# Kernel optimization log

Hardware: AMD Instinct MI355X
Metric: run time of the kernel (lower is better)

Reference implementation:

```python
import jax, jax.numpy as jnp
from jax import lax
import numpy as np

TAU = 10.0      # tauSr == tauRef
THR = 1.0       # theta
WIDTH = 1.0     # tauRho (surrogate width)
SCALE = 1.0     # scaleRho (surrogate scale)
DECAY = float(np.exp(-1.0 / TAU))


@jax.custom_vjp
def _heaviside(v):
    # spike = 1[v >= theta]
    return (v >= THR).astype(v.dtype)

def _heaviside_fwd(v):
    return _heaviside(v), v

def _heaviside_bwd(v, g):
    # SLAYER exponential surrogate pdf: scaleRho/tauRho * exp(-|v-theta|/tauRho)
    return (g * (SCALE / WIDTH) * jnp.exp(-jnp.abs(v - THR) / WIDTH),)

_heaviside.defvjp(_heaviside_fwd, _heaviside_bwd)


def _conv2d(x, w, pad):
    # x: (B, Cin, H, W), w: (Cout, Cin, kh, kw); SLAYER convs have no bias
    return lax.conv_general_dilated(
        x, w, window_strides=(1, 1), padding=[(pad, pad), (pad, pad)],
        dimension_numbers=("NCHW", "OIHW", "NCHW"))


def _sumpool(x, k):
    # SLAYER pool = sum over kxk window (times a learned scalar applied outside)
    B, C, H, W = x.shape
    return x.reshape(B, C, H // k, k, W // k, k).sum(axis=(3, 5))


def _psp(seq):
    # exponential synaptic (PSP) filter along time: s[t] = a*s[t-1] + x[t]
    a = jnp.asarray(DECAY, seq.dtype)
    def step(s, x_t):
        s = a * s + x_t
        return s, s
    _, out = lax.scan(step, jnp.zeros_like(seq[0]), seq)
    return out  # (T, ...)


def _spikes(u):
    # thresholded spiking with decaying refractory feedback (scaleRef=1):
    # v[t] = u[t] - r[t]; s[t] = 1[v >= theta]; r[t+1] = b*(r[t] + theta*s[t])
    b = jnp.asarray(DECAY, u.dtype)
    def step(r, u_t):
        s = _heaviside(u_t - r)
        r_next = b * (r + THR * s)
        return r_next, s
    _, out = lax.scan(step, jnp.zeros_like(u[0]), u)
    return out  # (T, ...)


def _forward(x, conv1_w, conv2_w, lin_w, w_pool1, w_pool2):
    N, T, C, H, W = x.shape  # (64, 100, 2, 32, 32)
    h = _conv2d(x.reshape(N * T, C, H, W), conv1_w, 2)        # (NT, 4, 32, 32)
    h = _sumpool(h, 4) * w_pool1                               # (NT, 4, 8, 8)
    h = h.reshape(N, T, 4, 8, 8).swapaxes(0, 1)                # (T, N, 4, 8, 8)
    s1 = _spikes(_psp(h))                                      # (T, N, 4, 8, 8)
    h2 = _conv2d(s1.reshape(T * N, 4, 8, 8), conv2_w, 1)       # (TN, 8, 8, 8)
    h2 = (_sumpool(h2, 2) * w_pool2).reshape(T, N, 8, 4, 4)    # (T, N, 8, 4, 4)
    s2 = _spikes(_psp(h2))                                     # (T, N, 8, 4, 4)
    # dense = full-spatial conv (2, 8, 4, 4) -> (N, T, 2)
    return jnp.einsum("tnchw,ochw->nto", s2, lin_w)


def setup_inputs() -> dict:
    key = jax.random.key(0)
    ks = jax.random.split(key, 4)
    x = (jax.random.uniform(ks[0], (64, 100, 2, 32, 32)) < 0.1).astype(jnp.float32)
    conv1_w = jax.random.normal(ks[1], (4, 2, 5, 5), jnp.float32) * 0.3
    conv2_w = jax.random.normal(ks[2], (8, 4, 3, 3), jnp.float32) * 0.3
    lin_w = jax.random.normal(ks[3], (2, 8, 4, 4), jnp.float32) * 0.3
    w_pool1 = jnp.float32(1.0 / 16.0)  # 1.1*theta / (16 * 1.1)
    w_pool2 = jnp.float32(1.0 / 4.0)   # 1.1*theta / (4 * 1.1)
    return {"x": x, "conv1_w": conv1_w, "conv2_w": conv2_w, "lin_w": lin_w,
            "w_pool1": w_pool1, "w_pool2": w_pool2}


def reference(x, conv1_w, conv2_w, lin_w, w_pool1, w_pool2):
    return _forward(x, conv1_w, conv2_w, lin_w, w_pool1, w_pool2)
```

## Files before the change

kernel.cpp:

```cpp
#include <hip/hip_runtime.h>


#define DECAY 0.9048374180359595f

__global__ __launch_bounds__(128) void k0_fold(const float* __restrict__ w1,
        const float* __restrict__ w2, const float* __restrict__ wp1,
        const float* __restrict__ wp2, float* __restrict__ wl1,
        float* __restrict__ wl2) {
    const int tid = threadIdx.x;
    const float p1 = wp1[0], p2 = wp2[0];
    for (int idx = tid; idx < 512; idx += 128) {
        const int f = idx & 7, c = (idx >> 3) & 3, e = (idx >> 5) & 7, cin = idx >> 8;
        const int cc = c * 2 + cin;
        int alo = e - 3; if (alo < 0) alo = 0;
        int ahi = e;     if (ahi > 4) ahi = 4;
        int blo = f - 3; if (blo < 0) blo = 0;
        int bhi = f;     if (bhi > 4) bhi = 4;
        float s = 0.f;
        for (int a = alo; a <= ahi; ++a)
            for (int b = blo; b <= bhi; ++b)
                s += w1[cc * 25 + a * 5 + b];
        wl1[(cin * 8 + e) * 32 + c * 8 + f] = s * p1;
    }
    for (int idx = tid; idx < 512; idx += 128) {
        const int c2 = idx & 7, f = (idx >> 3) & 3, e = (idx >> 5) & 3, cin = idx >> 7;
        int alo = e - 1; if (alo < 0) alo = 0;
        int ahi = e;     if (ahi > 2) ahi = 2;
        int blo = f - 1; if (blo < 0) blo = 0;
        int bhi = f;     if (bhi > 2) bhi = 2;
        float s = 0.f;
        for (int aa = alo; aa <= ahi; ++aa)
            for (int bb = blo; bb <= bhi; ++bb)
                s += w2[((c2 * 4 + cin) * 3 + aa) * 3 + bb];
        wl2[c2 * 68 + cin * 16 + e * 4 + f] = s * p2;
    }
}

__global__ __launch_bounds__(64) void k1(const float* __restrict__ x,
        const float* __restrict__ wg, float* __restrict__ u1) {
    __shared__ __align__(16) float xs[2 * 1296];
    __shared__ __align__(16) float wl[512];
    const int lane = threadIdx.x;
    const int frame = blockIdx.x;
    const int n = frame / 100, t = frame % 100;

    *(float4*)(wl + 4 * lane)       = *(const float4*)(wg + 4 * lane);
    *(float4*)(wl + 256 + 4 * lane) = *(const float4*)(wg + 256 + 4 * lane);

    #pragma unroll
    for (int m0 = 0; m0 < 128; m0 += 64) {
        const int m = m0 + lane;
        if (m < 72) {
            const int cin = m / 36, rem = m % 36;
            const int rr = rem / 9, q4 = rem % 9;
            const int pr = (rr == 0) ? 0 : (rr == 1) ? 9 : (rr == 2) ? 26 : 35;
            *(float4*)(xs + cin * 1296 + pr * 36 + q4 * 4) = make_float4(0.f, 0.f, 0.f, 0.f);
        }
    }
    #pragma unroll
    for (int m0 = 0; m0 < 192; m0 += 64) {
        const int m = m0 + lane;
        if (m < 144) {
            const int cin = m / 72, rem = m % 72;
            const int side = rem & 1, pr = rem >> 1;
            *(float2*)(xs + cin * 1296 + pr * 36 + side * 34) = make_float2(0.f, 0.f);
        }
    }
    const float4* xg = (const float4*)(x + (size_t)frame * 2048);
    #pragma unroll
    for (int q = 0; q < 8; ++q) {
        const int m = q * 64 + lane;
        const float4 v = xg[m];
        const int li = 4 * m;
        const int cin = li >> 10, row = (li >> 5) & 31, col = li & 31;
        const int r = row + 2;
        const int pr = (r & 3) * 9 + (r >> 2);
        float* d = xs + cin * 1296 + pr * 36 + col + 2;
        *(float2*)(d)     = make_float2(v.x, v.y);
        *(float2*)(d + 2) = make_float2(v.z, v.w);
    }
    __syncthreads();

    const int cp = lane >> 5;
    const int i  = (lane >> 2) & 7;
    const int jh = (lane >> 1) & 1;
    const int eh = lane & 1;

    float acc[2][4] = {{0.f, 0.f, 0.f, 0.f}, {0.f, 0.f, 0.f, 0.f}};
    const float* tb = xs + (i + eh) * 36 + jh * 16;
    #pragma unroll
    for (int cin = 0; cin < 2; ++cin) {
        #pragma unroll
        for (int et = 0; et < 4; ++et) {
            const int ro = cin * 1296 + et * 9 * 36;
            float xr[20];
            #pragma unroll
            for (int b = 0; b < 5; ++b)
                *(float4*)(xr + 4 * b) = *(const float4*)(tb + ro + 4 * b);
            float wv[16];
            const float* wp = wl + (cin * 8 + eh * 4 + et) * 32 + cp * 16;
            #pragma unroll
            for (int q = 0; q < 4; ++q)
                *(float4*)(wv + 4 * q) = *(const float4*)(wp + 4 * q);
            #pragma unroll
            for (int cl = 0; cl < 2; ++cl) {
                #pragma unroll
                for (int jj = 0; jj < 4; ++jj) {
                    const int o = 4 * jj;
                    acc[cl][jj] += xr[o]*wv[cl*8]     + xr[o+1]*wv[cl*8+1]
                                 + xr[o+2]*wv[cl*8+2] + xr[o+3]*wv[cl*8+3]
                                 + xr[o+4]*wv[cl*8+4] + xr[o+5]*wv[cl*8+5]
                                 + xr[o+6]*wv[cl*8+6] + xr[o+7]*wv[cl*8+7];
                }
            }
        }
    }
    #pragma unroll
    for (int cl = 0; cl < 2; ++cl)
        #pragma unroll
        for (int jj = 0; jj < 4; ++jj)
            acc[cl][jj] += __shfl_xor(acc[cl][jj], 1);

    const float o0 = eh ? acc[1][0] : acc[0][0];
    const float o1 = eh ? acc[1][1] : acc[0][1];
    const float o2 = eh ? acc[1][2] : acc[0][2];
    const float o3 = eh ? acc[1][3] : acc[0][3];
    *(float4*)(u1 + (size_t)t * 16384 + n * 256 + (2 * cp + eh) * 64 + i * 8 + jh * 4) =
        make_float4(o0, o1, o2, o3);
}

__global__ __launch_bounds__(64) void k2_scan(float* __restrict__ u) {
    const int id = blockIdx.x * 64 + threadIdx.x;
    const float a = DECAY;
    float* p = u + id;
    float v[100];
    #pragma unroll
    for (int k = 0; k < 100; ++k) v[k] = p[(size_t)k * 16384];
    float psp = 0.f, r = 0.f;
    #pragma unroll
    for (int k = 0; k < 100; ++k) {
        psp = a * psp + v[k];
        const float vv = psp - r;
        const float s = (vv >= 1.f) ? 1.f : 0.f;
        r = a * (r + s);
        p[(size_t)k * 16384] = s;
    }
}

__global__ __launch_bounds__(256) void k3(const float* __restrict__ s1,
        const float* __restrict__ wl2g, float* __restrict__ u2) {
    __shared__ __align__(16) float xs[8 * 660];
    __shared__ __align__(16) float wl[544];
    const int tid = threadIdx.x, sub = tid >> 5, l = tid & 31;

    for (int m = tid; m < 136; m += 256)
        *(float4*)(wl + 4 * m) = *(const float4*)(wl2g + 4 * m);

    float* xt = xs + sub * 660;
    float4* fz = (float4*)xt;
    for (int m = l; m < 160; m += 32) fz[m] = make_float4(0.f, 0.f, 0.f, 0.f);

    const int frame = blockIdx.x * 8 + sub;
    const int t = frame >> 6, n = frame & 63;
    const float* fr = s1 + (size_t)t * 16384 + n * 256;
    {
        const int cin = l >> 3, row = l & 7;
        const int r = row + 1;
        const int pr = (r & 1) * 5 + (r >> 1);
        const float4 v0 = *(const float4*)(fr + cin * 64 + row * 8);
        const float4 v1 = *(const float4*)(fr + cin * 64 + row * 8 + 4);
        *(float4*)(xt + cin * 160 + pr * 16 + 4) = v0;
        *(float4*)(xt + cin * 160 + pr * 16 + 8) = v1;
    }
    __syncthreads();

    const int c2 = l >> 2, i = l & 3;
    float acc[4] = {0.f, 0.f, 0.f, 0.f};
    const float* wb = wl + c2 * 68;
    const float* tb = xt + i * 16;
    #pragma unroll
    for (int cin = 0; cin < 4; ++cin) {
        #pragma unroll
        for (int e = 0; e < 4; ++e) {
            const int C = cin * 160 + ((e & 1) * 5 + (e >> 1)) * 16;
            float xr[16];
            #pragma unroll
            for (int b = 0; b < 4; ++b)
                *(float4*)(xr + 4 * b) = *(const float4*)(tb + C + 4 * b);
            float wv[4];
            *(float4*)(wv) = *(const float4*)(wb + cin * 16 + e * 4);
            #pragma unroll
            for (int j = 0; j < 4; ++j) {
                #pragma unroll
                for (int f = 0; f < 4; ++f)
                    acc[j] += xr[2 * j + f + 3] * wv[f];
            }
        }
    }
    *(float4*)(u2 + (size_t)t * 8192 + n * 128 + c2 * 16 + i * 4) =
        make_float4(acc[0], acc[1], acc[2], acc[3]);
}

__global__ __launch_bounds__(128, 2) void k45(const float* __restrict__ u2,
        const float* __restrict__ lw, float* __restrict__ out) {
    __shared__ float ls[25 * 128];
    const int f = threadIdx.x, n = blockIdx.x;
    const int wave = f >> 6, l = f & 63;
    const float a = DECAY;
    const float w0 = lw[l], w1v = lw[64 + l], w2v = lw[128 + l], w3v = lw[192 + l];
    float psp = 0.f, r = 0.f;
    const float* p = u2 + n * 128 + f;
    #pragma unroll 1
    for (int t0 = 0; t0 < 100; t0 += 25) {
        float v[25];
        #pragma unroll
        for (int k = 0; k < 25; ++k) v[k] = p[(size_t)(t0 + k) * 8192];
        #pragma unroll
        for (int k = 0; k < 25; ++k) {
            psp = a * psp + v[k];
            const float vv = psp - r;
            const float s = (vv >= 1.f) ? 1.f : 0.f;
            r = a * (r + s);
            ls[k * 128 + f] = s;
        }
        __syncthreads();
        const int base = wave ? 13 : 0, cnt = wave ? 12 : 13;
        for (int q = 0; q < cnt; ++q) {
            const int k = base + q;
            const float sa = ls[k * 128 + l], sb = ls[k * 128 + 64 + l];
            float a0 = sa * w0 + sb * w1v;
            float a1 = sa * w2v + sb * w3v;
            #pragma unroll
            for (int off = 32; off > 0; off >>= 1) {
                a0 += __shfl_down(a0, off);
                a1 += __shfl_down(a1, off);
            }
            if (l == 0) {
                const int tt = t0 + k;
                out[n * 200 + tt * 2]     = a0;
                out[n * 200 + tt * 2 + 1] = a1;
            }
        }
        __syncthreads();
    }
}

extern "C" void kernel_launch(void* const* d_in, const int* in_sizes, int n_in,
                              void* d_out, int out_size, void* d_ws, size_t ws_size,
                              hipStream_t stream) {
    const float* x   = (const float*)d_in[0];
    const float* w1  = (const float*)d_in[1];
    const float* w2  = (const float*)d_in[2];
    const float* lw  = (const float*)d_in[3];
    const float* wp1 = (const float*)d_in[4];
    const float* wp2 = (const float*)d_in[5];

    float* u1  = (float*)d_ws;
    float* u2  = u1 + 1638400;
    float* wl1 = u2 + 819200;
    float* wl2 = wl1 + 512;
    float* out = (float*)d_out;

    k0_fold<<<1, 128, 0, stream>>>(w1, w2, wp1, wp2, wl1, wl2);
    k1<<<6400, 64, 0, stream>>>(x, wl1, u1);
    k2_scan<<<256, 64, 0, stream>>>(u1);
    k3<<<800, 256, 0, stream>>>(u1, wl2, u2);
    k45<<<64, 128, 0, stream>>>(u2, lw, out);
}
```

Before: 140.6 us.

## Fuse first scan, second conv, second scan and dense layer into one kernel

Replaces k2_scan, k3 and k45 with a single kernel kf that runs one block per batch sample and walks time in chunks of 8 steps. In each chunk it computes the first PSP and spike scan, runs the 3x3 conv on spikes held in shared memory, then the second scan and the dense reduction. This removes the s1 write-back, the u2 round trip through global memory and two launches, and it prefetches the next chunk of u1 into registers. The cost is that the whole tail now runs on only 64 blocks with several barriers per chunk, so parallelism and latency hiding are much lower than in the 800-block conv kernel.

```diff
diff --git a/kernel.cpp b/kernel.cpp
--- a/kernel.cpp
+++ b/kernel.cpp
@@ -129,116 +129,126 @@
         make_float4(o0, o1, o2, o3);
 }
 
-__global__ __launch_bounds__(64) void k2_scan(float* __restrict__ u) {
-    const int id = blockIdx.x * 64 + threadIdx.x;
+__global__ __launch_bounds__(256) void kf(const float* __restrict__ u1,
+        const float* __restrict__ wl2g, const float* __restrict__ lw,
+        float* __restrict__ out) {
+    __shared__ __align__(16) float ls1[8 * 660];
+    __shared__ __align__(16) float ls2[8 * 132];
+    __shared__ __align__(16) float wl[544];
+    const int tid = threadIdx.x, n = blockIdx.x;
+    const int wave = tid >> 6, l64 = tid & 63;
+    const int sub = tid >> 5, l = tid & 31;
     const float a = DECAY;
-    float* p = u + id;
-    float v[100];
-    #pragma unroll
-    for (int k = 0; k < 100; ++k) v[k] = p[(size_t)k * 16384];
-    float psp = 0.f, r = 0.f;
-    #pragma unroll
-    for (int k = 0; k < 100; ++k) {
-        psp = a * psp + v[k];
-        const float vv = psp - r;
-        const float s = (vv >= 1.f) ? 1.f : 0.f;
-        r = a * (r + s);
-        p[(size_t)k * 16384] = s;
-    }
-}
-
-__global__ __launch_bounds__(256) void k3(const float* __restrict__ s1,
-        const float* __restrict__ wl2g, float* __restrict__ u2) {
-    __shared__ __align__(16) float xs[8 * 660];
-    __shared__ __align__(16) float wl[544];
-    const int tid = threadIdx.x, sub = tid >> 5, l = tid & 31;
-
-    for (int m = tid; m < 136; m += 256)
-        *(float4*)(wl + 4 * m) = *(const float4*)(wl2g + 4 * m);
-
-    float* xt = xs + sub * 660;
-    float4* fz = (float4*)xt;
-    for (int m = l; m < 160; m += 32) fz[m] = make_float4(0.f, 0.f, 0.f, 0.f);
-
-    const int frame = blockIdx.x * 8 + sub;
-    const int t = frame >> 6, n = frame & 63;
-    const float* fr = s1 + (size_t)t * 16384 + n * 256;
-    {
-        const int cin = l >> 3, row = l & 7;
-        const int r = row + 1;
-        const int pr = (r & 1) * 5 + (r >> 1);
-        const float4 v0 = *(const float4*)(fr + cin * 64 + row * 8);
-        const float4 v1 = *(const float4*)(fr + cin * 64 + row * 8 + 4);
-        *(float4*)(xt + cin * 160 + pr * 16 + 4) = v0;
-        *(float4*)(xt + cin * 160 + pr * 16 + 8) = v1;
-    }
+
+    if (tid < 136) *(float4*)(wl + 4 * tid) = *(const float4*)(wl2g + 4 * tid);
+    for (int m = tid; m < 1320; m += 256)
+        *(float4*)(ls1 + 4 * m) = make_float4(0.f, 0.f, 0.f, 0.f);
+
+    const int cs = tid >> 6, rowi = (tid >> 3) & 7, col = tid & 7;
+    const int pr1 = (((rowi + 1) & 1) * 5) + ((rowi + 1) >> 1);
+    const int woff = cs * 160 + pr1 * 16 + 4 + col;
+    const float* up = u1 + n * 256 + tid;
+
+    const int c2 = l >> 2, i2 = l & 3;
+    const float* wb = wl + c2 * 68;
+
+    const float dw0 = lw[l64], dw1 = lw[64 + l64], dw2 = lw[128 + l64], dw3 = lw[192 + l64];
+
+    float psp = 0.f, rr = 0.f;
+    float psp2 = 0.f, rr2 = 0.f;
+
+    float vbuf[8];
+    #pragma unroll
+    for (int k = 0; k < 8; ++k) vbuf[k] = up[(size_t)k * 16384];
+
     __syncthreads();
 
-    const int c2 = l >> 2, i = l & 3;
-    float acc[4] = {0.f, 0.f, 0.f, 0.f};
-    const float* wb = wl + c2 * 68;
-    const float* tb = xt + i * 16;
-    #pragma unroll
-    for (int cin = 0; cin < 4; ++cin) {
-        #pragma unroll
-        for (int e = 0; e < 4; ++e) {
-            const int C = cin * 160 + ((e & 1) * 5 + (e >> 1)) * 16;
-            float xr[16];
-            #pragma unroll
-            for (int b = 0; b < 4; ++b)
-                *(float4*)(xr + 4 * b) = *(const float4*)(tb + C + 4 * b);
-            float wv[4];
-            *(float4*)(wv) = *(const float4*)(wb + cin * 16 + e * 4);
-            #pragma unroll
-            for (int j = 0; j < 4; ++j) {
+    #pragma unroll 1
+    for (int rd = 0; rd < 13; ++rd) {
+        const int t0 = rd * 8;
+        const int cnt = (rd == 12) ? 4 : 8;
+
+        float sreg[8];
+        #pragma unroll
+        for (int k = 0; k < 8; ++k) {
+            if (k < cnt) {
+                psp = a * psp + vbuf[k];
+                const float vv = psp - rr;
+                const float s = (vv >= 1.f) ? 1.f : 0.f;
+                rr = a * (rr + s);
+                sreg[k] = s;
+            }
+        }
+        #pragma unroll
+        for (int k = 0; k < 8; ++k) {
+            const int tt = t0 + 8 + k;
+            if (tt < 100) vbuf[k] = up[(size_t)tt * 16384];
+        }
+        #pragma unroll
+        for (int k = 0; k < 8; ++k)
+            if (k < cnt) ls1[k * 660 + woff] = sreg[k];
+        __syncthreads();
+
+        if (sub < cnt) {
+            const float* tb = ls1 + sub * 660 + i2 * 16;
+            float acc[4] = {0.f, 0.f, 0.f, 0.f};
+            #pragma unroll
+            for (int cin = 0; cin < 4; ++cin) {
                 #pragma unroll
-                for (int f = 0; f < 4; ++f)
-                    acc[j] += xr[2 * j + f + 3] * wv[f];
-            }
-        }
-    }
-    *(float4*)(u2 + (size_t)t * 8192 + n * 128 + c2 * 16 + i * 4) =
-        make_float4(acc[0], acc[1], acc[2], acc[3]);
-}
-
-__global__ __launch_bounds__(128, 2) void k45(const float* __restrict__ u2,
-        const float* __restrict__ lw, float* __restrict__ out) {
-    __shared__ float ls[25 * 128];
-    const int f = threadIdx.x, n = blockIdx.x;
-    const int wave = f >> 6, l = f & 63;
-    const float a = DECAY;
-    const float w0 = lw[l], w1v = lw[64 + l], w2v = lw[128 + l], w3v = lw[192 + l];
-    float psp = 0.f, r = 0.f;
-    const float* p = u2 + n * 128 + f;
-    #pragma unroll 1
-    for (int t0 = 0; t0 < 100; t0 += 25) {
-        float v[25];
-        #pragma unroll
-        for (int k = 0; k < 25; ++k) v[k] = p[(size_t)(t0 + k) * 8192];
-        #pragma unroll
-        for (int k = 0; k < 25; ++k) {
-            psp = a * psp + v[k];
-            const float vv = psp - r;
-            const float s = (vv >= 1.f) ? 1.f : 0.f;
-            r = a * (r + s);
-            ls[k * 128 + f] = s;
-        }
-        __syncthreads();
-        const int base = wave ? 13 : 0, cnt = wave ? 12 : 13;
-        for (int q = 0; q < cnt; ++q) {
-            const int k = base + q;
-            const float sa = ls[k * 128 + l], sb = ls[k * 128 + 64 + l];
-            float a0 = sa * w0 + sb * w1v;
-            float a1 = sa * w2v + sb * w3v;
-            #pragma unroll
-            for (int off = 32; off > 0; off >>= 1) {
-                a0 += __shfl_down(a0, off);
-                a1 += __shfl_down(a1, off);
-            }
-            if (l == 0) {
-                const int tt = t0 + k;
-                out[n * 200 + tt * 2]     = a0;
-                out[n * 200 + tt * 2 + 1] = a1;
+                for (int e = 0; e < 4; ++e) {
+                    const int C = cin * 160 + ((e & 1) * 5 + (e >> 1)) * 16;
+                    float xr[16];
+                    #pragma unroll
+                    for (int b = 0; b < 4; ++b)
+                        *(float4*)(xr + 4 * b) = *(const float4*)(tb + C + 4 * b);
+                    float wv[4];
+                    *(float4*)(wv) = *(const float4*)(wb + cin * 16 + e * 4);
+                    #pragma unroll
+                    for (int j = 0; j < 4; ++j) {
+                        #pragma unroll
+                        for (int f = 0; f < 4; ++f)
+                            acc[j] += xr[2 * j + f + 3] * wv[f];
+                    }
+                }
+            }
+            *(float4*)(ls2 + sub * 132 + c2 * 16 + i2 * 4) =
+                make_float4(acc[0], acc[1], acc[2], acc[3]);
+        }
+        __syncthreads();
+
+        if (tid < 128) {
+            #pragma unroll
+            for (int k = 0; k < 8; ++k) {
+                if (k < cnt) {
+                    const float u = ls2[k * 132 + tid];
+                    psp2 = a * psp2 + u;
+                    const float vv = psp2 - rr2;
+                    const float s = (vv >= 1.f) ? 1.f : 0.f;
+                    rr2 = a * (rr2 + s);
+                    ls2[k * 132 + tid] = s;
+                }
+            }
+        }
+        __syncthreads();
+
+        #pragma unroll
+        for (int h = 0; h < 2; ++h) {
+            const int ss = wave + 4 * h;
+            if (ss < cnt) {
+                const float sa = ls2[ss * 132 + l64];
+                const float sb = ls2[ss * 132 + 64 + l64];
+                float a0 = sa * dw0 + sb * dw1;
+                float a1 = sa * dw2 + sb * dw3;
+                #pragma unroll
+                for (int off = 32; off > 0; off >>= 1) {
+                    a0 += __shfl_down(a0, off);
+                    a1 += __shfl_down(a1, off);
+                }
+                if (l64 == 0) {
+                    const int tt = t0 + ss;
+                    out[n * 200 + tt * 2]     = a0;
+                    out[n * 200 + tt * 2 + 1] = a1;
+                }
             }
         }
         __syncthreads();
@@ -256,14 +266,11 @@
     const float* wp2 = (const float*)d_in[5];
 
     float* u1  = (float*)d_ws;
-    float* u2  = u1 + 1638400;
-    float* wl1 = u2 + 819200;
+    float* wl1 = u1 + 1638400;
     float* wl2 = wl1 + 512;
     float* out = (float*)d_out;
 
     k0_fold<<<1, 128, 0, stream>>>(w1, w2, wp1, wp2, wl1, wl2);
     k1<<<6400, 64, 0, stream>>>(x, wl1, u1);
-    k2_scan<<<256, 64, 0, stream>>>(u1);
-    k3<<<800, 256, 0, stream>>>(u1, wl2, u2);
-    k45<<<64, 128, 0, stream>>>(u2, lw, out);
-}
+    kf<<<64, 256, 0, stream>>>(u1, wl2, lw, out);
+}
```

New measurement: 143.2 us. No clear change (+1.9%).
